# Performance work log

Measured on AMD Instinct MI355X. Metric: run time of the kernel, lower is better.

The kernel has to match this reference:

```python
import jax, jax.numpy as jnp
import numpy as np

# --- hashgrid config (from __init__: num_levels=16, level_dim=4, base_res=2, log2_hashmap_size=19, desired_res=2048) ---
NUM_LEVELS = 16
LEVEL_DIM = 4
BASE_RES = 2
DESIRED_RES = 2048
TABLE_SIZE = 2 ** 19
_b = np.exp((np.log(DESIRED_RES) - np.log(BASE_RES)) / (NUM_LEVELS - 1))
SCALES = BASE_RES * _b ** np.arange(NUM_LEVELS) - 1.0          # instant-ngp per-level scale
RES = (np.ceil(SCALES) + 1).astype(np.int64)                   # per-level grid resolution
PRIME = np.uint32(2654435761)                                  # 2D spatial hash prime


def softplus10(x):
    return jax.nn.softplus(10.0 * x) / 10.0


def hash_encode(u, tables):
    """u: [P,2] in [0,1]; tables: [L, TABLE_SIZE, LEVEL_DIM]. Returns [P, L*LEVEL_DIM]."""
    outs = []
    for l in range(NUM_LEVELS):
        s = float(SCALES[l])
        res = int(RES[l])
        pos = u * s + 0.5
        pf = jnp.floor(pos)
        fr = pos - pf                      # bilinear fractions, [P,2]
        pi = pf.astype(jnp.int32)
        acc = None
        for dx in (0, 1):
            for dy in (0, 1):
                cx = pi[:, 0] + dx
                cy = pi[:, 1] + dy
                if res * res <= TABLE_SIZE:
                    idx = cy * res + cx                                   # dense level
                else:
                    idx = (cx.astype(jnp.uint32) ^ (cy.astype(jnp.uint32) * PRIME)) % jnp.uint32(TABLE_SIZE)
                    idx = idx.astype(jnp.int32)                           # hashed level
                wx = fr[:, 0] if dx else 1.0 - fr[:, 0]
                wy = fr[:, 1] if dy else 1.0 - fr[:, 1]
                term = tables[l][idx] * (wx * wy)[:, None]                # gather + bilerp
                acc = term if acc is None else acc + term
        outs.append(acc)
    return jnp.concatenate(outs, axis=-1)


def setup_inputs() -> dict:
    key = jax.random.key(0)
    ks = jax.random.split(key, 4)
    B, N, T = 4, 2048, 192
    x = jax.random.normal(ks[0], (B, N, T, 2), jnp.float32)
    embeddings = jax.random.normal(ks[1], (NUM_LEVELS, TABLE_SIZE, LEVEL_DIM), jnp.float32) * 1e-2
    W0 = jax.random.normal(ks[2], (64, 64), jnp.float32) / 8.0
    b0 = jnp.zeros((64,), jnp.float32)
    W1 = jax.random.normal(ks[3], (64, 1), jnp.float32) / 8.0
    b1 = jnp.zeros((1,), jnp.float32)
    return {"x": x, "embeddings": embeddings, "W0": W0, "b0": b0, "W1": W1, "b1": b1}


def reference(x, embeddings, W0, b0, W1, b1):
    B, N, T = x.shape[:3]
    xf = x.reshape(-1, T, 2)                       # [B*N, T, 2]
    rays_o = xf[:, 0]
    rd = xf[:, -1] - xf[:, 0]
    rd = rd / jnp.linalg.norm(rd, axis=-1, keepdims=True)
    z = jnp.linspace(0.0, 2.0, T)                  # [T]
    sample_dist = 1.0 / T
    xys = rays_o[:, None, :] + rd[:, None, :] * z[None, :, None]   # [B*N, T, 2]
    xys = jnp.clip(xys, -1.0, 1.0)                 # aabb clamp [-1,-1,1,1]
    u = (xys.reshape(-1, 2) + 1.0) * 0.5           # map [-bound,bound] -> [0,1], bound=1
    feats = hash_encode(u, embeddings)             # [P, 64]
    h = softplus10(feats @ W0 + b0)
    sigma = softplus10(h @ W1 + b1).reshape(-1, T) # [B*N, T]
    deltas = jnp.concatenate([jnp.full((1,), sample_dist, sigma.dtype), z[1:] - z[:-1]])  # [T]
    density = (deltas[None, :] * sigma).reshape(B, N, T)
    return density
```

## Files before the change

### kernel.cpp

```cpp
#include <hip/hip_runtime.h>
#include <cmath>
#include <algorithm>

#define NUM_LEVELS 16
#define TABLE_SIZE 524288
#define TMASK (TABLE_SIZE - 1)
#define HASH_PRIME 2654435761u
#define T_SAMPLES 192
#define BLOCK 256
#define PTS 64
#define CHUNK 4096
#define N_RAYS 8192

typedef _Float16 f16;
typedef f16 f16x4 __attribute__((ext_vector_type(4)));
typedef f16 f16x8 __attribute__((ext_vector_type(8)));
typedef float f32x4 __attribute__((ext_vector_type(4)));

struct LvlParams {
    float s[NUM_LEVELS];
    int   res[NUM_LEVELS];
    int   mode[NUM_LEVELS];
    int   offB[NUM_LEVELS];
    int   used[NUM_LEVELS];
};

#define C_10L2E  14.42695040888963f
#define C_LN2_01 0.0693147180559945f

#define EXP2F(x) __builtin_amdgcn_exp2f(x)
#define LOG2F(x) __builtin_amdgcn_logf(x)

__device__ __constant__ const int LVL[4][4] = {
    {0, 1, 8, 13},
    {2, 3, 7, 14},
    {4, 5, 6, 15},
    {9, 10, 11, 12},
};

__device__ __forceinline__ f16x4 lerp4h(f16x4 c00, f16x4 c01, f16x4 c10, f16x4 c11,
                                        float fx, float fy) {
    float gx = 1.0f - fx, gy = 1.0f - fy;
    f16 w00 = (f16)(gx * gy), w01 = (f16)(gx * fy);
    f16 w10 = (f16)(fx * gy), w11 = (f16)(fx * fy);
    f16x4 v00 = {w00, w00, w00, w00}, v01 = {w01, w01, w01, w01};
    f16x4 v10 = {w10, w10, w10, w10}, v11 = {w11, w11, w11, w11};
    return c00 * v00 + c01 * v01 + c10 * v10 + c11 * v11;
}

__device__ __forceinline__ f16x4 lerp4f(f32x4 c00, f32x4 c01, f32x4 c10, f32x4 c11,
                                        float fx, float fy) {
    float w00 = (1.0f - fx) * (1.0f - fy), w01 = (1.0f - fx) * fy;
    float w10 = fx * (1.0f - fy),          w11 = fx * fy;
    f32x4 a = c00 * w00 + c01 * w01 + c10 * w10 + c11 * w11;
    return __builtin_convertvector(a, f16x4);
}

__global__ void prep_tables(const float* __restrict__ emb, char* __restrict__ embq,
                            const float* __restrict__ W0, f16* __restrict__ w0f,
                            const float* __restrict__ x, float* __restrict__ rayBuf,
                            const LvlParams lp) {
    const int t = threadIdx.x;
    if (blockIdx.x == 0 && blockIdx.y == 0) {
        #pragma unroll
        for (int i = 0; i < 16; ++i) {
            int f = t * 16 + i;
            int j = f & 7, lx = (f >> 3) & 15, q = (f >> 7) & 3, nt = (f >> 9) & 3, kc = f >> 11;
            w0f[f] = (f16)W0[(kc * 32 + q * 8 + j) * 64 + (nt * 16 + lx)];
        }
    }
    if (blockIdx.y == 1 && blockIdx.x < (N_RAYS / 256)) {
        const int ray = blockIdx.x * 256 + t;
        const float2 o  = *(const float2*)(x + (size_t)ray * (T_SAMPLES * 2));
        const float2 ep = *(const float2*)(x + (size_t)ray * (T_SAMPLES * 2) + (T_SAMPLES - 1) * 2);
        float rdx = ep.x - o.x, rdy = ep.y - o.y;
        float inv = 1.0f / sqrtf(rdx * rdx + rdy * rdy);
        f32x4 rb; rb.x = o.x; rb.y = o.y; rb.z = rdx * inv; rb.w = rdy * inv;
        *(f32x4*)(rayBuf + (size_t)ray * 4) = rb;
    }
    const int l    = blockIdx.y;
    const int used = lp.used[l];
    const int base = blockIdx.x * CHUNK;
    if (base >= used) return;
    const float* src = emb + (size_t)l * TABLE_SIZE * 4;
    char* dst = embq + lp.offB[l];
    if (lp.mode[l] == 1) {
        const int res = lp.res[l];
        #pragma unroll
        for (int i = 0; i < 16; ++i) {
            int e = base + t + 256 * i;
            if (e < used) {
                f32x4 v00 = *(const f32x4*)(src + (size_t)e * 4);
                f32x4 v10 = *(const f32x4*)(src + (size_t)(e + 1) * 4);
                f32x4 v01 = *(const f32x4*)(src + (size_t)(e + res) * 4);
                f32x4 v11 = *(const f32x4*)(src + (size_t)(e + res + 1) * 4);
                f16x4 a = __builtin_convertvector(v00, f16x4);
                f16x4 b = __builtin_convertvector(v10, f16x4);
                f16x4 c = __builtin_convertvector(v01, f16x4);
                f16x4 d = __builtin_convertvector(v11, f16x4);
                f16x8 q0 = __builtin_shufflevector(a, b, 0, 1, 2, 3, 4, 5, 6, 7);
                f16x8 q1 = __builtin_shufflevector(c, d, 0, 1, 2, 3, 4, 5, 6, 7);
                *(f16x8*)(dst + ((size_t)e << 5))      = q0;
                *(f16x8*)(dst + ((size_t)e << 5) + 16) = q1;
            }
        }
    } else {
        #pragma unroll
        for (int i = 0; i < 16; ++i) {
            int e = base + t + 256 * i;
            if (e < used) {
                f32x4 v = *(const f32x4*)(src + (size_t)e * 4);
                *(f16x4*)(dst + (size_t)e * 8) = __builtin_convertvector(v, f16x4);
            }
        }
    }
}

template<bool QT>
__launch_bounds__(BLOCK, 8)
__global__ void nerf_fused(const float* __restrict__ x,
                           const float* __restrict__ emb,
                           const char* __restrict__ embq,
                           const f16* __restrict__ w0f,
                           const float* __restrict__ rayBuf,
                           const float* __restrict__ b0,
                           const float* __restrict__ W1,
                           const float* __restrict__ b1,
                           float* __restrict__ out,
                           const LvlParams lp) {
    __shared__ __align__(16) f16 feT2[8 * PTS * 8];
    __shared__ __align__(16) f16 w0lds[4096];

    const int tid  = threadIdx.x;
    const int lane = tid & 63;
    const int w    = __builtin_amdgcn_readfirstlane(tid >> 6);

    f16x8 wreg0, wreg1;
    {
        const f16x8* wp = (const f16x8*)(w0f + (size_t)tid * 16);
        wreg0 = wp[0]; wreg1 = wp[1];
    }

    const int ray = blockIdx.x / 3;
    const int t   = (blockIdx.x - ray * 3) * PTS + lane;
    const float z = (float)((double)t * (2.0 / 191.0));

    float ux, uy;
    if (QT) {
        const f32x4 rb = *(const f32x4*)(rayBuf + (size_t)ray * 4);
        float px = fminf(fmaxf(rb.x + rb.z * z, -1.0f), 1.0f);
        float py = fminf(fmaxf(rb.y + rb.w * z, -1.0f), 1.0f);
        ux = (px + 1.0f) * 0.5f;
        uy = (py + 1.0f) * 0.5f;
    } else {
        const float2 o  = *(const float2*)(x + (size_t)ray * (T_SAMPLES * 2));
        const float2 ep = *(const float2*)(x + (size_t)ray * (T_SAMPLES * 2) + (T_SAMPLES - 1) * 2);
        float rdx = ep.x - o.x, rdy = ep.y - o.y;
        float inv = 1.0f / sqrtf(rdx * rdx + rdy * rdy);
        rdx *= inv; rdy *= inv;
        float px = fminf(fmaxf(o.x + rdx * z, -1.0f), 1.0f);
        float py = fminf(fmaxf(o.y + rdy * z, -1.0f), 1.0f);
        ux = (px + 1.0f) * 0.5f;
        uy = (py + 1.0f) * 0.5f;
    }

    if (QT) {
        f16x4 c00[4], c01[4], c10[4], c11[4];
        float fxs[4], fys[4];
        #pragma unroll
        for (int li = 0; li < 4; ++li) {
            const int l = LVL[w][li];
            const int mode = lp.mode[l];
            const float s = lp.s[l];
            float posx = ux * s + 0.5f, posy = uy * s + 0.5f;
            float pfx = floorf(posx), pfy = floorf(posy);
            fxs[li] = posx - pfx; fys[li] = posy - pfy;
            int cx = (int)pfx, cy = (int)pfy;
            const char* lb = embq + lp.offB[l];
            if (mode == 2) {
                unsigned hy0 = (unsigned)cy * HASH_PRIME;
                unsigned hy1 = hy0 + HASH_PRIME;
                int iA  = (int)(((unsigned)cx ^ hy0) & TMASK);
                int iB  = (int)(((unsigned)cx ^ hy1) & TMASK);
                int iA1 = (int)(((unsigned)(cx + 1) ^ hy0) & TMASK);
                int iB1 = (int)(((unsigned)(cx + 1) ^ hy1) & TMASK);
                c00[li] = *(const f16x4*)(lb + ((size_t)iA  << 3));
                c01[li] = *(const f16x4*)(lb + ((size_t)iB  << 3));
                c10[li] = *(const f16x4*)(lb + ((size_t)iA1 << 3));
                c11[li] = *(const f16x4*)(lb + ((size_t)iB1 << 3));
            } else if (mode == 1) {
                int i00 = cy * lp.res[l] + cx;
                f16x8 q0 = *(const f16x8*)(lb + ((size_t)i00 << 5));
                f16x8 q1 = *(const f16x8*)(lb + ((size_t)i00 << 5) + 16);
                c00[li] = __builtin_shufflevector(q0, q0, 0, 1, 2, 3);
                c10[li] = __builtin_shufflevector(q0, q0, 4, 5, 6, 7);
                c01[li] = __builtin_shufflevector(q1, q1, 0, 1, 2, 3);
                c11[li] = __builtin_shufflevector(q1, q1, 4, 5, 6, 7);
            } else {
                const int res = lp.res[l];
                int i00 = cy * res + cx;
                const f16x4* tb = (const f16x4*)lb;
                c00[li] = tb[i00];       c10[li] = tb[i00 + 1];
                c01[li] = tb[i00 + res]; c11[li] = tb[i00 + res + 1];
            }
        }
        {
            f16x8* wl = (f16x8*)&w0lds[(size_t)tid * 16];
            wl[0] = wreg0; wl[1] = wreg1;
        }
        #pragma unroll
        for (int li = 0; li < 4; ++li) {
            const int l = LVL[w][li];
            f16x4 r = lerp4h(c00[li], c01[li], c10[li], c11[li], fxs[li], fys[li]);
            *(f16x4*)&feT2[(((l >> 1) * PTS + lane) * 8) + (l & 1) * 4] = r;
        }
    } else {
        {
            f16x8* wl = (f16x8*)&w0lds[(size_t)tid * 16];
            wl[0] = wreg0; wl[1] = wreg1;
        }
        #pragma unroll
        for (int li = 0; li < 4; ++li) {
            const int l = LVL[w][li];
            const float s = lp.s[l];
            float posx = ux * s + 0.5f, posy = uy * s + 0.5f;
            float pfx = floorf(posx), pfy = floorf(posy);
            float fx = posx - pfx, fy = posy - pfy;
            int cx = (int)pfx, cy = (int)pfy;
            int i00, i01, i10, i11;
            if (lp.mode[l] == 2) {
                unsigned hy0 = (unsigned)cy * HASH_PRIME;
                unsigned hy1 = hy0 + HASH_PRIME;
                i00 = (int)(((unsigned)cx ^ hy0) & TMASK);
                i01 = (int)(((unsigned)cx ^ hy1) & TMASK);
                i10 = (int)(((unsigned)(cx + 1) ^ hy0) & TMASK);
                i11 = (int)(((unsigned)(cx + 1) ^ hy1) & TMASK);
            } else {
                const int res = lp.res[l];
                i00 = cy * res + cx; i10 = i00 + 1;
                i01 = i00 + res;     i11 = i01 + 1;
            }
            const f32x4* tb = (const f32x4*)(emb + (size_t)l * (TABLE_SIZE * 4));
            f32x4 a = tb[i00], b = tb[i01], c = tb[i10], d = tb[i11];
            f16x4 r = lerp4f(a, b, c, d, fx, fy);
            *(f16x4*)&feT2[(((l >> 1) * PTS + lane) * 8) + (l & 1) * 4] = r;
        }
    }

    const int lx = lane & 15, q = lane >> 4;
    float b0l2[4], w1l2[4];
    #pragma unroll
    for (int nt = 0; nt < 4; ++nt) {
        b0l2[nt] = b0[nt * 16 + lx] * C_10L2E;
        w1l2[nt] = W1[nt * 16 + lx] * C_LN2_01;
    }
    const float b1v = b1[0];

    __syncthreads();

    const int p = w * 16 + lx;

    f32x4 acc[4];
    #pragma unroll
    for (int nt = 0; nt < 4; ++nt) acc[nt] = (f32x4)(0.0f);

    #pragma unroll
    for (int kc = 0; kc < 2; ++kc) {
        f16x8 afr = *(const f16x8*)&feT2[((kc * 4 + q) * PTS + p) * 8];
        #pragma unroll
        for (int nt = 0; nt < 4; ++nt) {
            f16x8 bfr = *(const f16x8*)&w0lds[(size_t)(((kc * 4 + nt) * 4 + q) * 16 + lx) * 8];
            acc[nt] = __builtin_amdgcn_mfma_f32_16x16x32_f16(afr, bfr, acc[nt], 0, 0, 0);
        }
    }

    const float d0 = (float)(1.0 / 192.0);
    const float d1 = (float)(2.0 / 191.0);

    float part[4];
    #pragma unroll
    for (int r = 0; r < 4; ++r) {
        float pp = 0.0f;
        #pragma unroll
        for (int nt = 0; nt < 4; ++nt) {
            float t2 = fmaf(acc[nt][r], C_10L2E, b0l2[nt]);
            float e2 = EXP2F(-fabsf(t2));
            float sp = fmaxf(t2, 0.0f) + LOG2F(1.0f + e2);
            pp = fmaf(sp, w1l2[nt], pp);
        }
        pp += __shfl_xor(pp, 1, 64);
        pp += __shfl_xor(pp, 2, 64);
        pp += __shfl_xor(pp, 4, 64);
        pp += __shfl_xor(pp, 8, 64);
        part[r] = pp;
    }
    if (lx == 0) {
        const int g0 = blockIdx.x * PTS + w * 16 + q * 4;
        const int tt = g0 % T_SAMPLES;
        const float dd0 = d0 * C_LN2_01, dd1 = d1 * C_LN2_01;
        f32x4 ov;
        #pragma unroll
        for (int r = 0; r < 4; ++r) {
            float t2 = (part[r] + b1v) * C_10L2E;
            float e2 = EXP2F(-fabsf(t2));
            float sp = fmaxf(t2, 0.0f) + LOG2F(1.0f + e2);
            ov[r] = sp * ((r == 0 && tt == 0) ? dd0 : dd1);
        }
        *(f32x4*)(out + g0) = ov;
    }
}

extern "C" void kernel_launch(void* const* d_in, const int* in_sizes, int n_in,
                              void* d_out, int out_size, void* d_ws, size_t ws_size,
                              hipStream_t stream) {
    const float* x   = (const float*)d_in[0];
    const float* emb = (const float*)d_in[1];
    const float* W0  = (const float*)d_in[2];
    const float* b0  = (const float*)d_in[3];
    const float* W1  = (const float*)d_in[4];
    const float* b1  = (const float*)d_in[5];
    float* out = (float*)d_out;

    char*  ws     = (char*)d_ws;
    f16*   w0f    = (f16*)ws;
    float* rayBuf = (float*)(ws + 8192);
    char*  embq   = ws + 147456;

    LvlParams lp;
    const double bb = std::exp((std::log(2048.0) - std::log(2.0)) / 15.0);
    int offB = 0, maxUsed = 0;
    for (int l = 0; l < NUM_LEVELS; ++l) {
        double sc = 2.0 * std::pow(bb, (double)l) - 1.0;
        int rr = (int)std::ceil(sc) + 1;
        lp.s[l] = (float)sc;
        lp.res[l] = rr;
        const bool hashed = ((long long)rr * (long long)rr > (long long)TABLE_SIZE);
        int used;
        if (hashed) {
            used = TABLE_SIZE;
        } else {
            long long cmax = (long long)std::floor(sc + 0.5) + 1;
            long long u = cmax * (long long)rr + cmax + 1 + (rr + 2);
            used = (int)std::min((long long)TABLE_SIZE, u);
        }
        lp.mode[l] = hashed ? 2 : (rr >= 150 ? 1 : 0);
        lp.offB[l] = offB;
        lp.used[l] = used;
        const long long bytes = (lp.mode[l] == 1) ? (long long)used * 32
                                                  : (long long)used * 8;
        offB += (int)((bytes + 4095) & ~4095LL);
        if (used > maxUsed) maxUsed = used;
    }
    const size_t need = 147456 + (size_t)offB;
    const bool useQ = ws_size >= need;

    const int nblk = out_size / PTS;
    if (useQ) {
        dim3 pg((maxUsed + CHUNK - 1) / CHUNK, NUM_LEVELS);
        prep_tables<<<pg, 256, 0, stream>>>(emb, embq, W0, w0f, x, rayBuf, lp);
        nerf_fused<true><<<nblk, BLOCK, 0, stream>>>(x, emb, embq, w0f, rayBuf,
                                                     b0, W1, b1, out, lp);
    } else {
        dim3 pg1(1, 1);
        prep_tables<<<pg1, 256, 0, stream>>>(emb, embq, W0, w0f, x, rayBuf, lp);
        nerf_fused<false><<<nblk, BLOCK, 0, stream>>>(x, emb, embq, w0f, rayBuf,
                                                      b0, W1, b1, out, lp);
    }
}
```

Measured before the change: 324.9 us.

## Process a whole ray per block and overlap next-tile gathers with MFMA

Each block now handles all 192 samples of one ray as three 64-point tiles instead of one tile per block. While the MFMA and epilogue run for the current tile, the hash-table gathers for the next tile's levels are already in flight, using manual barriers between stages. The per-block setup (W0 staging to LDS, bias loads, ray params) is paid once per ray rather than three times. The cost is three times fewer blocks, higher register pressure from held gather results, and extra barriers.

```diff
diff --git a/kernel.cpp b/kernel.cpp
--- a/kernel.cpp
+++ b/kernel.cpp
@@ -30,6 +30,9 @@
 
 #define EXP2F(x) __builtin_amdgcn_exp2f(x)
 #define LOG2F(x) __builtin_amdgcn_logf(x)
+
+#define BARRIER() do { asm volatile("s_waitcnt lgkmcnt(0)" ::: "memory"); \
+                       __builtin_amdgcn_s_barrier(); } while (0)
 
 __device__ __constant__ const int LVL[4][4] = {
     {0, 1, 8, 13},
@@ -141,110 +144,17 @@
         wreg0 = wp[0]; wreg1 = wp[1];
     }
 
-    const int ray = blockIdx.x / 3;
-    const int t   = (blockIdx.x - ray * 3) * PTS + lane;
-    const float z = (float)((double)t * (2.0 / 191.0));
-
-    float ux, uy;
+    const int ray = blockIdx.x;
+
+    f32x4 rb;
     if (QT) {
-        const f32x4 rb = *(const f32x4*)(rayBuf + (size_t)ray * 4);
-        float px = fminf(fmaxf(rb.x + rb.z * z, -1.0f), 1.0f);
-        float py = fminf(fmaxf(rb.y + rb.w * z, -1.0f), 1.0f);
-        ux = (px + 1.0f) * 0.5f;
-        uy = (py + 1.0f) * 0.5f;
+        rb = *(const f32x4*)(rayBuf + (size_t)ray * 4);
     } else {
         const float2 o  = *(const float2*)(x + (size_t)ray * (T_SAMPLES * 2));
         const float2 ep = *(const float2*)(x + (size_t)ray * (T_SAMPLES * 2) + (T_SAMPLES - 1) * 2);
         float rdx = ep.x - o.x, rdy = ep.y - o.y;
         float inv = 1.0f / sqrtf(rdx * rdx + rdy * rdy);
-        rdx *= inv; rdy *= inv;
-        float px = fminf(fmaxf(o.x + rdx * z, -1.0f), 1.0f);
-        float py = fminf(fmaxf(o.y + rdy * z, -1.0f), 1.0f);
-        ux = (px + 1.0f) * 0.5f;
-        uy = (py + 1.0f) * 0.5f;
-    }
-
-    if (QT) {
-        f16x4 c00[4], c01[4], c10[4], c11[4];
-        float fxs[4], fys[4];
-        #pragma unroll
-        for (int li = 0; li < 4; ++li) {
-            const int l = LVL[w][li];
-            const int mode = lp.mode[l];
-            const float s = lp.s[l];
-            float posx = ux * s + 0.5f, posy = uy * s + 0.5f;
-            float pfx = floorf(posx), pfy = floorf(posy);
-            fxs[li] = posx - pfx; fys[li] = posy - pfy;
-            int cx = (int)pfx, cy = (int)pfy;
-            const char* lb = embq + lp.offB[l];
-            if (mode == 2) {
-                unsigned hy0 = (unsigned)cy * HASH_PRIME;
-                unsigned hy1 = hy0 + HASH_PRIME;
-                int iA  = (int)(((unsigned)cx ^ hy0) & TMASK);
-                int iB  = (int)(((unsigned)cx ^ hy1) & TMASK);
-                int iA1 = (int)(((unsigned)(cx + 1) ^ hy0) & TMASK);
-                int iB1 = (int)(((unsigned)(cx + 1) ^ hy1) & TMASK);
-                c00[li] = *(const f16x4*)(lb + ((size_t)iA  << 3));
-                c01[li] = *(const f16x4*)(lb + ((size_t)iB  << 3));
-                c10[li] = *(const f16x4*)(lb + ((size_t)iA1 << 3));
-                c11[li] = *(const f16x4*)(lb + ((size_t)iB1 << 3));
-            } else if (mode == 1) {
-                int i00 = cy * lp.res[l] + cx;
-                f16x8 q0 = *(const f16x8*)(lb + ((size_t)i00 << 5));
-                f16x8 q1 = *(const f16x8*)(lb + ((size_t)i00 << 5) + 16);
-                c00[li] = __builtin_shufflevector(q0, q0, 0, 1, 2, 3);
-                c10[li] = __builtin_shufflevector(q0, q0, 4, 5, 6, 7);
-                c01[li] = __builtin_shufflevector(q1, q1, 0, 1, 2, 3);
-                c11[li] = __builtin_shufflevector(q1, q1, 4, 5, 6, 7);
-            } else {
-                const int res = lp.res[l];
-                int i00 = cy * res + cx;
-                const f16x4* tb = (const f16x4*)lb;
-                c00[li] = tb[i00];       c10[li] = tb[i00 + 1];
-                c01[li] = tb[i00 + res]; c11[li] = tb[i00 + res + 1];
-            }
-        }
-        {
-            f16x8* wl = (f16x8*)&w0lds[(size_t)tid * 16];
-            wl[0] = wreg0; wl[1] = wreg1;
-        }
-        #pragma unroll
-        for (int li = 0; li < 4; ++li) {
-            const int l = LVL[w][li];
-            f16x4 r = lerp4h(c00[li], c01[li], c10[li], c11[li], fxs[li], fys[li]);
-            *(f16x4*)&feT2[(((l >> 1) * PTS + lane) * 8) + (l & 1) * 4] = r;
-        }
-    } else {
-        {
-            f16x8* wl = (f16x8*)&w0lds[(size_t)tid * 16];
-            wl[0] = wreg0; wl[1] = wreg1;
-        }
-        #pragma unroll
-        for (int li = 0; li < 4; ++li) {
-            const int l = LVL[w][li];
-            const float s = lp.s[l];
-            float posx = ux * s + 0.5f, posy = uy * s + 0.5f;
-            float pfx = floorf(posx), pfy = floorf(posy);
-            float fx = posx - pfx, fy = posy - pfy;
-            int cx = (int)pfx, cy = (int)pfy;
-            int i00, i01, i10, i11;
-            if (lp.mode[l] == 2) {
-                unsigned hy0 = (unsigned)cy * HASH_PRIME;
-                unsigned hy1 = hy0 + HASH_PRIME;
-                i00 = (int)(((unsigned)cx ^ hy0) & TMASK);
-                i01 = (int)(((unsigned)cx ^ hy1) & TMASK);
-                i10 = (int)(((unsigned)(cx + 1) ^ hy0) & TMASK);
-                i11 = (int)(((unsigned)(cx + 1) ^ hy1) & TMASK);
-            } else {
-                const int res = lp.res[l];
-                i00 = cy * res + cx; i10 = i00 + 1;
-                i01 = i00 + res;     i11 = i01 + 1;
-            }
-            const f32x4* tb = (const f32x4*)(emb + (size_t)l * (TABLE_SIZE * 4));
-            f32x4 a = tb[i00], b = tb[i01], c = tb[i10], d = tb[i11];
-            f16x4 r = lerp4f(a, b, c, d, fx, fy);
-            *(f16x4*)&feT2[(((l >> 1) * PTS + lane) * 8) + (l & 1) * 4] = r;
-        }
+        rb.x = o.x; rb.y = o.y; rb.z = rdx * inv; rb.w = rdy * inv;
     }
 
     const int lx = lane & 15, q = lane >> 4;
@@ -255,59 +165,173 @@
         w1l2[nt] = W1[nt * 16 + lx] * C_LN2_01;
     }
     const float b1v = b1[0];
-
-    __syncthreads();
-
     const int p = w * 16 + lx;
 
-    f32x4 acc[4];
-    #pragma unroll
-    for (int nt = 0; nt < 4; ++nt) acc[nt] = (f32x4)(0.0f);
-
-    #pragma unroll
-    for (int kc = 0; kc < 2; ++kc) {
-        f16x8 afr = *(const f16x8*)&feT2[((kc * 4 + q) * PTS + p) * 8];
-        #pragma unroll
-        for (int nt = 0; nt < 4; ++nt) {
-            f16x8 bfr = *(const f16x8*)&w0lds[(size_t)(((kc * 4 + nt) * 4 + q) * 16 + lx) * 8];
-            acc[nt] = __builtin_amdgcn_mfma_f32_16x16x32_f16(afr, bfr, acc[nt], 0, 0, 0);
-        }
-    }
-
-    const float d0 = (float)(1.0 / 192.0);
-    const float d1 = (float)(2.0 / 191.0);
-
-    float part[4];
-    #pragma unroll
-    for (int r = 0; r < 4; ++r) {
-        float pp = 0.0f;
-        #pragma unroll
-        for (int nt = 0; nt < 4; ++nt) {
-            float t2 = fmaf(acc[nt][r], C_10L2E, b0l2[nt]);
-            float e2 = EXP2F(-fabsf(t2));
-            float sp = fmaxf(t2, 0.0f) + LOG2F(1.0f + e2);
-            pp = fmaf(sp, w1l2[nt], pp);
-        }
-        pp += __shfl_xor(pp, 1, 64);
-        pp += __shfl_xor(pp, 2, 64);
-        pp += __shfl_xor(pp, 4, 64);
-        pp += __shfl_xor(pp, 8, 64);
-        part[r] = pp;
-    }
-    if (lx == 0) {
-        const int g0 = blockIdx.x * PTS + w * 16 + q * 4;
-        const int tt = g0 % T_SAMPLES;
-        const float dd0 = d0 * C_LN2_01, dd1 = d1 * C_LN2_01;
-        f32x4 ov;
+    auto mfma_epi = [&](int tileIdx) {
+        f32x4 acc[4];
+        #pragma unroll
+        for (int nt = 0; nt < 4; ++nt) acc[nt] = (f32x4)(0.0f);
+        #pragma unroll
+        for (int kc = 0; kc < 2; ++kc) {
+            f16x8 afr = *(const f16x8*)&feT2[((kc * 4 + q) * PTS + p) * 8];
+            #pragma unroll
+            for (int nt = 0; nt < 4; ++nt) {
+                f16x8 bfr = *(const f16x8*)&w0lds[(size_t)(((kc * 4 + nt) * 4 + q) * 16 + lx) * 8];
+                acc[nt] = __builtin_amdgcn_mfma_f32_16x16x32_f16(afr, bfr, acc[nt], 0, 0, 0);
+            }
+        }
+        const float d0 = (float)(1.0 / 192.0);
+        const float d1 = (float)(2.0 / 191.0);
+        float part[4];
         #pragma unroll
         for (int r = 0; r < 4; ++r) {
-            float t2 = (part[r] + b1v) * C_10L2E;
-            float e2 = EXP2F(-fabsf(t2));
-            float sp = fmaxf(t2, 0.0f) + LOG2F(1.0f + e2);
-            ov[r] = sp * ((r == 0 && tt == 0) ? dd0 : dd1);
-        }
-        *(f32x4*)(out + g0) = ov;
-    }
+            float pp = 0.0f;
+            #pragma unroll
+            for (int nt = 0; nt < 4; ++nt) {
+                float t2 = fmaf(acc[nt][r], C_10L2E, b0l2[nt]);
+                float e2 = EXP2F(-fabsf(t2));
+                float sp = fmaxf(t2, 0.0f) + LOG2F(1.0f + e2);
+                pp = fmaf(sp, w1l2[nt], pp);
+            }
+            pp += __shfl_xor(pp, 1, 64);
+            pp += __shfl_xor(pp, 2, 64);
+            pp += __shfl_xor(pp, 4, 64);
+            pp += __shfl_xor(pp, 8, 64);
+            part[r] = pp;
+        }
+        if (lx == 0) {
+            const int tt0 = tileIdx * PTS + w * 16 + q * 4;
+            const int g0  = ray * T_SAMPLES + tt0;
+            const float dd0 = d0 * C_LN2_01, dd1 = d1 * C_LN2_01;
+            f32x4 ov;
+            #pragma unroll
+            for (int r = 0; r < 4; ++r) {
+                float t2 = (part[r] + b1v) * C_10L2E;
+                float e2 = EXP2F(-fabsf(t2));
+                float sp = fmaxf(t2, 0.0f) + LOG2F(1.0f + e2);
+                ov[r] = sp * ((r == 0 && tt0 == 0) ? dd0 : dd1);
+            }
+            *(f32x4*)(out + g0) = ov;
+        }
+    };
+
+    float ux, uy;
+    f16x4 c00[4], c01[4], c10[4], c11[4];
+    float fxs[4], fys[4];
+
+#define U_SETUP(IT)                                                         \
+    {   const float z = (float)((double)((IT) * PTS + lane) * (2.0 / 191.0)); \
+        float px = fminf(fmaxf(rb.x + rb.z * z, -1.0f), 1.0f);              \
+        float py = fminf(fmaxf(rb.y + rb.w * z, -1.0f), 1.0f);              \
+        ux = (px + 1.0f) * 0.5f; uy = (py + 1.0f) * 0.5f; }
+
+#define ISSUE_LEVEL(LI)                                                     \
+    {   const int l = LVL[w][LI];                                           \
+        const int mode = lp.mode[l];                                        \
+        const float s = lp.s[l];                                            \
+        float posx = ux * s + 0.5f, posy = uy * s + 0.5f;                   \
+        float pfx = floorf(posx), pfy = floorf(posy);                       \
+        fxs[LI] = posx - pfx; fys[LI] = posy - pfy;                         \
+        int cx = (int)pfx, cy = (int)pfy;                                   \
+        const char* lb = embq + lp.offB[l];                                 \
+        if (mode == 2) {                                                    \
+            unsigned hy0 = (unsigned)cy * HASH_PRIME;                       \
+            unsigned hy1 = hy0 + HASH_PRIME;                                \
+            int iA  = (int)(((unsigned)cx ^ hy0) & TMASK);                  \
+            int iB  = (int)(((unsigned)cx ^ hy1) & TMASK);                  \
+            int iA1 = (int)(((unsigned)(cx + 1) ^ hy0) & TMASK);            \
+            int iB1 = (int)(((unsigned)(cx + 1) ^ hy1) & TMASK);            \
+            c00[LI] = *(const f16x4*)(lb + ((size_t)iA  << 3));             \
+            c01[LI] = *(const f16x4*)(lb + ((size_t)iB  << 3));             \
+            c10[LI] = *(const f16x4*)(lb + ((size_t)iA1 << 3));             \
+            c11[LI] = *(const f16x4*)(lb + ((size_t)iB1 << 3));             \
+        } else if (mode == 1) {                                             \
+            int i00 = cy * lp.res[l] + cx;                                  \
+            f16x8 q0 = *(const f16x8*)(lb + ((size_t)i00 << 5));            \
+            f16x8 q1 = *(const f16x8*)(lb + ((size_t)i00 << 5) + 16);       \
+            c00[LI] = __builtin_shufflevector(q0, q0, 0, 1, 2, 3);          \
+            c10[LI] = __builtin_shufflevector(q0, q0, 4, 5, 6, 7);          \
+            c01[LI] = __builtin_shufflevector(q1, q1, 0, 1, 2, 3);          \
+            c11[LI] = __builtin_shufflevector(q1, q1, 4, 5, 6, 7);          \
+        } else {                                                            \
+            const int res = lp.res[l];                                      \
+            int i00 = cy * res + cx;                                        \
+            const f16x4* tb = (const f16x4*)lb;                             \
+            c00[LI] = tb[i00];       c10[LI] = tb[i00 + 1];                 \
+            c01[LI] = tb[i00 + res]; c11[LI] = tb[i00 + res + 1];           \
+        }                                                                   \
+    }
+
+#define LERP_LEVEL(LI)                                                      \
+    {   const int l = LVL[w][LI];                                           \
+        f16x4 r = lerp4h(c00[LI], c01[LI], c10[LI], c11[LI], fxs[LI], fys[LI]); \
+        *(f16x4*)&feT2[(((l >> 1) * PTS + lane) * 8) + (l & 1) * 4] = r; }
+
+    if (QT) {
+        U_SETUP(0)
+        ISSUE_LEVEL(0) ISSUE_LEVEL(1) ISSUE_LEVEL(2) ISSUE_LEVEL(3)
+        {
+            f16x8* wl = (f16x8*)&w0lds[(size_t)tid * 16];
+            wl[0] = wreg0; wl[1] = wreg1;
+        }
+        LERP_LEVEL(0) LERP_LEVEL(1) LERP_LEVEL(2) LERP_LEVEL(3)
+        U_SETUP(1)
+        ISSUE_LEVEL(2) ISSUE_LEVEL(3)
+        BARRIER();
+        mfma_epi(0);
+        BARRIER();
+        ISSUE_LEVEL(0) ISSUE_LEVEL(1)
+        LERP_LEVEL(2) LERP_LEVEL(3) LERP_LEVEL(0) LERP_LEVEL(1)
+        U_SETUP(2)
+        ISSUE_LEVEL(2) ISSUE_LEVEL(3)
+        BARRIER();
+        mfma_epi(1);
+        BARRIER();
+        ISSUE_LEVEL(0) ISSUE_LEVEL(1)
+        LERP_LEVEL(2) LERP_LEVEL(3) LERP_LEVEL(0) LERP_LEVEL(1)
+        BARRIER();
+        mfma_epi(2);
+    } else {
+        {
+            f16x8* wl = (f16x8*)&w0lds[(size_t)tid * 16];
+            wl[0] = wreg0; wl[1] = wreg1;
+        }
+        for (int it = 0; it < 3; ++it) {
+            U_SETUP(it)
+            #pragma unroll
+            for (int li = 0; li < 4; ++li) {
+                const int l = LVL[w][li];
+                const float s = lp.s[l];
+                float posx = ux * s + 0.5f, posy = uy * s + 0.5f;
+                float pfx = floorf(posx), pfy = floorf(posy);
+                float fx = posx - pfx, fy = posy - pfy;
+                int cx = (int)pfx, cy = (int)pfy;
+                int i00, i01, i10, i11;
+                if (lp.mode[l] == 2) {
+                    unsigned hy0 = (unsigned)cy * HASH_PRIME;
+                    unsigned hy1 = hy0 + HASH_PRIME;
+                    i00 = (int)(((unsigned)cx ^ hy0) & TMASK);
+                    i01 = (int)(((unsigned)cx ^ hy1) & TMASK);
+                    i10 = (int)(((unsigned)(cx + 1) ^ hy0) & TMASK);
+                    i11 = (int)(((unsigned)(cx + 1) ^ hy1) & TMASK);
+                } else {
+                    const int res = lp.res[l];
+                    i00 = cy * res + cx; i10 = i00 + 1;
+                    i01 = i00 + res;     i11 = i01 + 1;
+                }
+                const f32x4* tb = (const f32x4*)(emb + (size_t)l * (TABLE_SIZE * 4));
+                f32x4 a = tb[i00], b = tb[i01], c = tb[i10], d = tb[i11];
+                f16x4 r = lerp4f(a, b, c, d, fx, fy);
+                *(f16x4*)&feT2[(((l >> 1) * PTS + lane) * 8) + (l & 1) * 4] = r;
+            }
+            BARRIER();
+            mfma_epi(it);
+            BARRIER();
+        }
+    }
+#undef U_SETUP
+#undef ISSUE_LEVEL
+#undef LERP_LEVEL
 }
 
 extern "C" void kernel_launch(void* const* d_in, const int* in_sizes, int n_in,
@@ -354,7 +378,7 @@
     const size_t need = 147456 + (size_t)offB;
     const bool useQ = ws_size >= need;
 
-    const int nblk = out_size / PTS;
+    const int nblk = out_size / T_SAMPLES;
     if (useQ) {
         dim3 pg((maxUsed + CHUNK - 1) / CHUNK, NUM_LEVELS);
         prep_tables<<<pg, 256, 0, stream>>>(emb, embq, W0, w0f, x, rayBuf, lp);
```

After: 374.8 us. 1.15x slower.
